# Performance work log

Measured on AMD Instinct MI355X. Metric: run time of the kernel, lower is better.

The kernel has to match this reference:

```python
import jax, jax.numpy as jnp
import numpy as np

B, M, F, E = 64, 1024, 4, 256      # batch, memory length, tokens-per-memory-cell, emb_size
NW, HOPS, PL = 32000, 3, 128       # vocab, hops, profile_len


def _embed(table, idx):
    # nn.Embedding with padding_idx=0 -> index 0 maps to zero vector
    return table[idx] * (idx != 0)[..., None].astype(table.dtype)


def _gru_step(x, h, Wih, Whh, bih, bhh):
    # single-step PyTorch GRU cell
    gi = x @ Wih.T + bih
    gh = h @ Whh.T + bhh
    ir, iz, i_n = jnp.split(gi, 3, axis=-1)
    hr, hz, h_n = jnp.split(gh, 3, axis=-1)
    r = jax.nn.sigmoid(ir + hr)
    z = jax.nn.sigmoid(iz + hz)
    n = jnp.tanh(i_n + r * h_n)
    return (1.0 - z) * n + z * h


def setup_inputs() -> dict:
    key = jax.random.key(0)
    ks = jax.random.split(key, 13)
    # HOPS+1 unique embedding tables: A[0..hops-1] plus C[hops-1]; C[h]=tables[h+1] (weight tying)
    tables = (jax.random.normal(ks[0], (HOPS + 1, NW, E)) * 0.1).at[:, 0, :].set(0.0)
    s = 1.0 / np.sqrt(E)
    Wih = jax.random.uniform(ks[1], (3 * E, E), minval=-s, maxval=s)
    Whh = jax.random.uniform(ks[2], (3 * E, E), minval=-s, maxval=s)
    bih = jax.random.uniform(ks[3], (3 * E,), minval=-s, maxval=s)
    bhh = jax.random.uniform(ks[4], (3 * E,), minval=-s, maxval=s)
    sp = 1.0 / np.sqrt(PL)
    Wp = jax.random.uniform(ks[5], (E, PL), minval=-sp, maxval=sp)
    bp = jax.random.uniform(ks[6], (E,), minval=-sp, maxval=sp)
    sv = 1.0 / np.sqrt(2 * E)
    Wv = jax.random.uniform(ks[7], (NW, 2 * E), minval=-sv, maxval=sv)
    bv = jax.random.uniform(ks[8], (NW,), minval=-sv, maxval=sv)
    context = jax.random.randint(ks[9], (B, M, F), 0, NW)
    y_ = jax.random.randint(ks[10], (B,), 0, NW)
    h_ = jax.random.normal(ks[11], (1, B, E))
    profile_encoding = jax.random.normal(ks[12], (B, PL))
    return dict(tables=tables, Wih=Wih, Whh=Whh, bih=bih, bhh=bhh, Wp=Wp, bp=bp,
                Wv=Wv, bv=bv, context=context, y_=y_, h_=h_,
                profile_encoding=profile_encoding)


def reference(tables, Wih, Whh, bih, bhh, Wp, bp, Wv, bv, context, y_, h_, profile_encoding):
    # load_memory (eval mode: no word dropout): memories[h] = sum over F of table[h] embeddings
    ctx = context.reshape(B, M * F)
    mems = [_embed(tables[hop], ctx).reshape(B, M, F, E).sum(axis=2) for hop in range(HOPS + 1)]
    # decoder step
    m = _embed(tables[1], y_)                    # C[0](y_)
    h = _gru_step(m, h_[0], Wih, Whh, bih, bhh)  # [B, E]
    q = h
    p = p_vocab = p_resto = None
    for hop in range(HOPS):
        p_ = mems[hop] * q[:, None, :]           # [B, M, E] elementwise attention scores
        p = p_.sum(axis=2)                        # [B, M]
        attn = jax.nn.softmax(p, axis=1)
        o = jnp.einsum('bm,bme->be', attn, mems[hop + 1])
        if hop == 0:
            p_vocab = jnp.concatenate([h, o], axis=1) @ Wv.T + bv  # uses q[0]=h
        if hop == 1:
            enc = profile_encoding @ Wp.T + bp   # [B, E]
            p_resto = jnp.einsum('bme,be->bm', p_, enc)
        q = q + o
    return p, p_vocab, p_resto, h[None]          # p_ptr, p_vocab, p_resto, h [1,B,E]
```

## Files before the change

### kernel.cpp

```cpp
#include <hip/hip_runtime.h>
#include <cstdint>

#define B_ 64
#define M_ 1024
#define F_ 4
#define E_ 256
#define NW_ 32000
#define PL_ 128

#define P_OFF   0
#define PV_OFF  65536
#define PR_OFF  2113536
#define H_OFF   2179072

typedef unsigned short u16;
typedef unsigned int u32;

typedef __bf16 bf16x8 __attribute__((ext_vector_type(8)));
typedef float f32x4 __attribute__((ext_vector_type(4)));

__device__ __forceinline__ u16 f2bf(float f) {
    u32 x = __builtin_bit_cast(u32, f);
    u32 r = (x + 0x7fffu + ((x >> 16) & 1u)) >> 16;
    return (u16)r;
}
__device__ __forceinline__ float bflo(u32 v) {
    return __builtin_bit_cast(float, v << 16);
}
__device__ __forceinline__ float bfhi(u32 v) {
    return __builtin_bit_cast(float, v & 0xffff0000u);
}
__device__ __forceinline__ float dot8(uint4 u, float4 qa, float4 qb) {
    return bflo(u.x) * qa.x + bfhi(u.x) * qa.y + bflo(u.y) * qa.z + bfhi(u.y) * qa.w +
           bflo(u.z) * qb.x + bfhi(u.z) * qb.y + bflo(u.w) * qb.z + bfhi(u.w) * qb.w;
}
__device__ __forceinline__ void acc8(uint4 u, float* a) {
    a[0] += bflo(u.x); a[1] += bfhi(u.x); a[2] += bflo(u.y); a[3] += bfhi(u.y);
    a[4] += bflo(u.z); a[5] += bfhi(u.z); a[6] += bflo(u.w); a[7] += bfhi(u.w);
}
__device__ __forceinline__ uint4 pack8(const float* s) {
    uint4 u;
    u.x = (u32)f2bf(s[0]) | ((u32)f2bf(s[1]) << 16);
    u.y = (u32)f2bf(s[2]) | ((u32)f2bf(s[3]) << 16);
    u.z = (u32)f2bf(s[4]) | ((u32)f2bf(s[5]) << 16);
    u.w = (u32)f2bf(s[6]) | ((u32)f2bf(s[7]) << 16);
    return u;
}
__device__ __forceinline__ bf16x8 pack_bf8(float4 a, float4 b) {
    union { u16 s[8]; bf16x8 v; } u;
    u.s[0] = f2bf(a.x); u.s[1] = f2bf(a.y); u.s[2] = f2bf(a.z); u.s[3] = f2bf(a.w);
    u.s[4] = f2bf(b.x); u.s[5] = f2bf(b.y); u.s[6] = f2bf(b.z); u.s[7] = f2bf(b.w);
    return u.v;
}

__global__ __launch_bounds__(256) void k_conv(
    const float* __restrict__ tables, u16* __restrict__ t0b, u16* __restrict__ t12)
{
    int t = blockIdx.y;
    int c = blockIdx.x * 256 + threadIdx.x;
    const float* src = tables + (size_t)t * NW_ * E_ + (size_t)c * 8;
    float4 a = *(const float4*)src;
    float4 b = *(const float4*)(src + 4);
    float s[8] = {a.x, a.y, a.z, a.w, b.x, b.y, b.z, b.w};
    uint4 u = pack8(s);
    if (t == 0) {
        *(uint4*)(t0b + (size_t)c * 8) = u;
    } else {
        int row = c >> 5, e = (c & 31) * 8;
        *(uint4*)(t12 + (size_t)row * 512 + (t - 1) * 256 + e) = u;
    }
}

__global__ __launch_bounds__(256) void k_gru(
    const float* __restrict__ tables, const float* __restrict__ Wih,
    const float* __restrict__ Whh, const float* __restrict__ bih,
    const float* __restrict__ bhh, const float* __restrict__ Wp,
    const float* __restrict__ bp, const int* __restrict__ y,
    const float* __restrict__ h_, const float* __restrict__ pe,
    float* __restrict__ q0, float* __restrict__ enc, float* __restrict__ outh)
{
    int b = blockIdx.x, t = threadIdx.x;
    __shared__ float m_s[E_], h_s[E_], pe_s[PL_];
    int yb = y[b];
    m_s[t] = tables[(size_t)NW_ * E_ + (size_t)yb * E_ + t];
    h_s[t] = h_[b * E_ + t];
    if (t < PL_) pe_s[t] = pe[b * PL_ + t];
    __syncthreads();

    float g_i[3], g_h[3];
#pragma unroll
    for (int g = 0; g < 3; g++) {
        int j = g * E_ + t;
        float ai = bih[j], ah = bhh[j];
        const float4* wi = (const float4*)(Wih + (size_t)j * E_);
        const float4* wh = (const float4*)(Whh + (size_t)j * E_);
#pragma unroll 8
        for (int e = 0; e < E_ / 4; e++) {
            float4 a = wi[e], c = wh[e];
            ai += a.x * m_s[4 * e] + a.y * m_s[4 * e + 1] +
                  a.z * m_s[4 * e + 2] + a.w * m_s[4 * e + 3];
            ah += c.x * h_s[4 * e] + c.y * h_s[4 * e + 1] +
                  c.z * h_s[4 * e + 2] + c.w * h_s[4 * e + 3];
        }
        g_i[g] = ai; g_h[g] = ah;
    }
    float r = 1.f / (1.f + expf(-(g_i[0] + g_h[0])));
    float z = 1.f / (1.f + expf(-(g_i[1] + g_h[1])));
    float n = tanhf(g_i[2] + r * g_h[2]);
    float hv = (1.f - z) * n + z * h_s[t];
    q0[b * E_ + t] = hv;
    outh[b * E_ + t] = hv;

    float ea = bp[t];
    const float4* wp = (const float4*)(Wp + (size_t)t * PL_);
#pragma unroll 8
    for (int p = 0; p < PL_ / 4; p++) {
        float4 a = wp[p];
        ea += a.x * pe_s[4 * p] + a.y * pe_s[4 * p + 1] +
              a.z * pe_s[4 * p + 2] + a.w * pe_s[4 * p + 3];
    }
    enc[b * E_ + t] = ea;
}

__global__ __launch_bounds__(256) void k_scores0(
    const u16* __restrict__ t0b, const int* __restrict__ ctx,
    const float* __restrict__ q, float* __restrict__ p_ws)
{
    int b = blockIdx.y, grp = blockIdx.x;
    int lane = threadIdx.x & 63, w = threadIdx.x >> 6;
    int h = lane >> 5, l32 = lane & 31, e0 = l32 * 8;
    float4 qa = *(const float4*)(q + b * E_ + e0);
    float4 qb = *(const float4*)(q + b * E_ + e0 + 4);
    int mbase = grp * 32 + w * 8;
    const int4* cp = (const int4*)(ctx + ((size_t)b * M_ + mbase) * 4);
    int4 c[8];
#pragma unroll
    for (int i = 0; i < 8; i++) c[i] = cp[i];

    float pa[8];
#pragma unroll
    for (int i = 0; i < 8; i++) {
        int ia = h ? c[i].y : c[i].x;
        int ib = h ? c[i].w : c[i].z;
        uint4 ra = *(const uint4*)(t0b + (size_t)ia * E_ + e0);
        uint4 rb = *(const uint4*)(t0b + (size_t)ib * E_ + e0);
        pa[i] = dot8(ra, qa, qb) + dot8(rb, qa, qb);
    }
#pragma unroll
    for (int o = 32; o > 0; o >>= 1)
#pragma unroll
        for (int i = 0; i < 8; i++) pa[i] += __shfl_xor(pa[i], o, 64);
    if (lane == 0)
#pragma unroll
        for (int i = 0; i < 8; i++) p_ws[(size_t)b * M_ + mbase + i] = pa[i];
}

__global__ __launch_bounds__(256) void k_soft(
    float* __restrict__ p_ws, const float* __restrict__ qcur,
    float* __restrict__ qnext)
{
    int b = blockIdx.x, t = threadIdx.x;
    __shared__ float red[256];
    float4 v = *(const float4*)(p_ws + (size_t)b * M_ + t * 4);
    float lm = fmaxf(fmaxf(v.x, v.y), fmaxf(v.z, v.w));
    red[t] = lm;
    __syncthreads();
    for (int s = 128; s > 0; s >>= 1) {
        if (t < s) red[t] = fmaxf(red[t], red[t + s]);
        __syncthreads();
    }
    float mx = red[0];
    __syncthreads();
    float e0 = expf(v.x - mx), e1 = expf(v.y - mx);
    float e2 = expf(v.z - mx), e3 = expf(v.w - mx);
    red[t] = e0 + e1 + e2 + e3;
    __syncthreads();
    for (int s = 128; s > 0; s >>= 1) {
        if (t < s) red[t] += red[t + s];
        __syncthreads();
    }
    float inv = 1.f / red[0];
    float4 o = make_float4(e0 * inv, e1 * inv, e2 * inv, e3 * inv);
    *(float4*)(p_ws + (size_t)b * M_ + t * 4) = o;
    qnext[b * E_ + t] = qcur[b * E_ + t];
}

__global__ __launch_bounds__(256) void k_mems12(
    const u16* __restrict__ t12, const int* __restrict__ ctx,
    const float* __restrict__ attn0, u16* __restrict__ mems1,
    u16* __restrict__ mems2, float* __restrict__ q1)
{
    int b = blockIdx.y, grp = blockIdx.x;
    int lane = threadIdx.x & 63, w = threadIdx.x >> 6;
    int h = lane >> 5, l32 = lane & 31, e0 = l32 * 8;
    int mbase = grp * 32 + w * 8;
    const int4* cp = (const int4*)(ctx + ((size_t)b * M_ + mbase) * 4);
    int4 c[8];
#pragma unroll
    for (int i = 0; i < 8; i++) c[i] = cp[i];
    float4 a01 = *(const float4*)(attn0 + (size_t)b * M_ + mbase);
    float4 a23 = *(const float4*)(attn0 + (size_t)b * M_ + mbase + 4);
    float wg[8] = {a01.x, a01.y, a01.z, a01.w, a23.x, a23.y, a23.z, a23.w};

    u16* mout = h ? mems2 : mems1;
    float o_acc[8] = {0, 0, 0, 0, 0, 0, 0, 0};
#pragma unroll
    for (int i = 0; i < 8; i++) {
        size_t off = (size_t)h * 256 + e0;
        uint4 r0 = *(const uint4*)(t12 + (size_t)c[i].x * 512 + off);
        uint4 r1 = *(const uint4*)(t12 + (size_t)c[i].y * 512 + off);
        uint4 r2 = *(const uint4*)(t12 + (size_t)c[i].z * 512 + off);
        uint4 r3 = *(const uint4*)(t12 + (size_t)c[i].w * 512 + off);
        float acc[8] = {0, 0, 0, 0, 0, 0, 0, 0};
        acc8(r0, acc); acc8(r1, acc); acc8(r2, acc); acc8(r3, acc);
        *(uint4*)(mout + ((size_t)(b * M_ + mbase + i)) * 256 + e0) = pack8(acc);
        if (h == 0) {
            float wgt = wg[i];
#pragma unroll
            for (int j = 0; j < 8; j++) o_acc[j] += wgt * acc[j];
        }
    }
    __shared__ float red[4][E_];
    if (h == 0)
#pragma unroll
        for (int j = 0; j < 8; j++) red[w][e0 + j] = o_acc[j];
    __syncthreads();
    int t = threadIdx.x;
    float s = red[0][t] + red[1][t] + red[2][t] + red[3][t];
    atomicAdd(q1 + b * E_ + t, s);
}

template <int MODE>
__global__ __launch_bounds__(256) void k_sscores(
    const u16* __restrict__ mems, const float* __restrict__ q,
    const float* __restrict__ enc, float* __restrict__ p_ws,
    float* __restrict__ out)
{
    int b = blockIdx.y, grp = blockIdx.x;
    int lane = threadIdx.x & 63, w = threadIdx.x >> 6;
    int h = lane >> 5, l32 = lane & 31, e0 = l32 * 8;
    float4 qa = *(const float4*)(q + b * E_ + e0);
    float4 qb = *(const float4*)(q + b * E_ + e0 + 4);
    float4 ea4 = make_float4(0, 0, 0, 0), eb4 = make_float4(0, 0, 0, 0);
    if (MODE == 1) {
        float4 ev = *(const float4*)(enc + b * E_ + e0);
        float4 ew = *(const float4*)(enc + b * E_ + e0 + 4);
        ea4 = make_float4(qa.x * ev.x, qa.y * ev.y, qa.z * ev.z, qa.w * ev.w);
        eb4 = make_float4(qb.x * ew.x, qb.y * ew.y, qb.z * ew.z, qb.w * ew.w);
    }
    int mbase = grp * 32 + w * 8;
    float pa[4], pr[4];
#pragma unroll
    for (int i = 0; i < 4; i++) {
        int m = mbase + 2 * i + h;
        uint4 r = *(const uint4*)(mems + ((size_t)(b * M_ + m)) * 256 + e0);
        pa[i] = dot8(r, qa, qb);
        if (MODE == 1) pr[i] = dot8(r, ea4, eb4);
    }
#pragma unroll
    for (int o = 16; o > 0; o >>= 1)
#pragma unroll
        for (int i = 0; i < 4; i++) {
            pa[i] += __shfl_xor(pa[i], o, 64);
            if (MODE == 1) pr[i] += __shfl_xor(pr[i], o, 64);
        }
    if (l32 == 0) {
#pragma unroll
        for (int i = 0; i < 4; i++) {
            int m = mbase + 2 * i + h;
            if (MODE == 2) out[P_OFF + (size_t)b * M_ + m] = pa[i];
            else           p_ws[(size_t)b * M_ + m] = pa[i];
            if (MODE == 1) out[PR_OFF + (size_t)b * M_ + m] = pr[i];
        }
    }
}

__global__ __launch_bounds__(256) void k_so(
    const u16* __restrict__ mems, const float* __restrict__ attn,
    float* __restrict__ qnext)
{
    int b = blockIdx.y, ch = blockIdx.x;
    int lane = threadIdx.x & 63, w = threadIdx.x >> 6;
    int h = lane >> 5, l32 = lane & 31, e0 = l32 * 8;
    int m0 = ch * 128;
    float acc[8] = {0, 0, 0, 0, 0, 0, 0, 0};
    for (int i = 0; i < 16; i++) {
        int m = m0 + i * 8 + w * 2 + h;
        float wgt = attn[(size_t)b * M_ + m];
        uint4 r = *(const uint4*)(mems + ((size_t)(b * M_ + m)) * 256 + e0);
        acc[0] += wgt * bflo(r.x); acc[1] += wgt * bfhi(r.x);
        acc[2] += wgt * bflo(r.y); acc[3] += wgt * bfhi(r.y);
        acc[4] += wgt * bflo(r.z); acc[5] += wgt * bfhi(r.z);
        acc[6] += wgt * bflo(r.w); acc[7] += wgt * bfhi(r.w);
    }
    __shared__ float red[8][E_];
    int hw = threadIdx.x >> 5;
#pragma unroll
    for (int j = 0; j < 8; j++) red[hw][e0 + j] = acc[j];
    __syncthreads();
    int t = threadIdx.x;
    float s = 0.f;
#pragma unroll
    for (int k = 0; k < 8; k++) s += red[k][t];
    atomicAdd(qnext + b * E_ + t, s);
}

__global__ __launch_bounds__(256) void k_pvocab(
    const float* __restrict__ Wv, const float* __restrict__ bv,
    const float* __restrict__ q0, const float* __restrict__ q1,
    float* __restrict__ out)
{
    __shared__ u16 X[64 * 512];
    int t = threadIdx.x;
#pragma unroll
    for (int it = 0; it < 16; it++) {
        int id = t + it * 256;
        int bb = id >> 6, c = id & 63;
        float v[8];
        if (c < 32) {
            const float* s = q0 + bb * E_ + c * 8;
#pragma unroll
            for (int j = 0; j < 8; j++) v[j] = s[j];
        } else {
            const float* s1 = q1 + bb * E_ + (c - 32) * 8;
            const float* s0 = q0 + bb * E_ + (c - 32) * 8;
#pragma unroll
            for (int j = 0; j < 8; j++) v[j] = s1[j] - s0[j];
        }
        uint4 uv = pack8(v);
        *(uint4*)(&X[bb * 512 + ((c ^ (bb & 7)) << 3)]) = uv;
    }
    __syncthreads();

    int lane = t & 63, w = t >> 6;
    int n0 = blockIdx.x * 128 + w * 32;
    int l15 = lane & 15, quad = lane >> 4;
    f32x4 acc[4][2];
#pragma unroll
    for (int mt = 0; mt < 4; mt++)
#pragma unroll
        for (int nt = 0; nt < 2; nt++)
            acc[mt][nt] = f32x4{0.f, 0.f, 0.f, 0.f};

    for (int ks = 0; ks < 16; ks++) {
        bf16x8 a[4], bfr[2];
#pragma unroll
        for (int mt = 0; mt < 4; mt++) {
            int m = mt * 16 + l15;
            int c = ks * 4 + quad;
            a[mt] = *(const bf16x8*)(&X[m * 512 + ((c ^ (m & 7)) << 3)]);
        }
#pragma unroll
        for (int nt = 0; nt < 2; nt++) {
            int n = n0 + nt * 16 + l15;
            const float4* wp = (const float4*)(Wv + (size_t)n * 512 + ks * 32 + quad * 8);
            bfr[nt] = pack_bf8(wp[0], wp[1]);
        }
#pragma unroll
        for (int mt = 0; mt < 4; mt++)
#pragma unroll
            for (int nt = 0; nt < 2; nt++)
                acc[mt][nt] = __builtin_amdgcn_mfma_f32_16x16x32_bf16(
                    a[mt], bfr[nt], acc[mt][nt], 0, 0, 0);
    }
#pragma unroll
    for (int nt = 0; nt < 2; nt++) {
        int n = n0 + nt * 16 + l15;
        float bvv = bv[n];
#pragma unroll
        for (int mt = 0; mt < 4; mt++) {
#pragma unroll
            for (int j = 0; j < 4; j++) {
                int m = mt * 16 + quad * 4 + j;
                out[PV_OFF + (size_t)m * 32000 + n] = acc[mt][nt][j] + bvv;
            }
        }
    }
}

extern "C" void kernel_launch(void* const* d_in, const int* in_sizes, int n_in,
                              void* d_out, int out_size, void* d_ws, size_t ws_size,
                              hipStream_t stream)
{
    const float* tables = (const float*)d_in[0];
    const float* Wih = (const float*)d_in[1];
    const float* Whh = (const float*)d_in[2];
    const float* bih = (const float*)d_in[3];
    const float* bhh = (const float*)d_in[4];
    const float* Wp  = (const float*)d_in[5];
    const float* bp  = (const float*)d_in[6];
    const float* Wv  = (const float*)d_in[7];
    const float* bv  = (const float*)d_in[8];
    const int* ctx = (const int*)d_in[9];
    const int* y   = (const int*)d_in[10];
    const float* h_  = (const float*)d_in[11];
    const float* pe  = (const float*)d_in[12];
    float* out = (float*)d_out;

    float* Wf   = (float*)d_ws;
    float* q    = Wf;
    float* enc  = Wf + 65536;
    float* p_ws = Wf + 81920;
    char* base  = (char*)d_ws + 589824;
    u16* t0b    = (u16*)base;
    u16* t12    = (u16*)(base + 16384000);
    u16* mems1  = (u16*)(base + 16384000 + 32768000);
    u16* mems2  = (u16*)(base + 16384000 + 32768000 + 33554432);

    k_conv<<<dim3(4000, 3), 256, 0, stream>>>(tables, t0b, t12);
    k_gru<<<64, 256, 0, stream>>>(tables, Wih, Whh, bih, bhh, Wp, bp, y, h_, pe,
                                  q, enc, out + H_OFF);
    k_scores0<<<dim3(32, 64), 256, 0, stream>>>(t0b, ctx, q, p_ws);
    k_soft<<<64, 256, 0, stream>>>(p_ws, q, q + 16384);
    k_mems12<<<dim3(32, 64), 256, 0, stream>>>(t12, ctx, p_ws, mems1, mems2,
                                               q + 16384);
    k_sscores<1><<<dim3(32, 64), 256, 0, stream>>>(mems1, q + 16384, enc, p_ws, out);
    k_soft<<<64, 256, 0, stream>>>(p_ws, q + 16384, q + 32768);
    k_so<<<dim3(8, 64), 256, 0, stream>>>(mems2, p_ws, q + 32768);
    k_sscores<2><<<dim3(32, 64), 256, 0, stream>>>(mems2, q + 32768, enc, p_ws, out);
    k_pvocab<<<250, 256, 0, stream>>>(Wv, bv, q, q + 16384, out);
}
```

Measured before the change: 399.5 us.

## Merge independent kernels into shared launches via block-index dispatch

Folds the table-conversion kernel and the GRU kernel into one launch whose first 64 blocks run the GRU and whose remaining blocks convert tables. Also merges the p_vocab MFMA GEMM into the hop-1 scores kernel, so the two independent pieces of work run concurrently in one grid. This removes two launches and lets small, low-occupancy kernels overlap with bandwidth-bound work. The cost is that the combined kernels carry the larger LDS footprint of the GEMM path, which may lower occupancy for the score blocks.

New measurement: 370.3 us. 1.08x faster.

```diff
diff --git a/kernel.cpp b/kernel.cpp
--- a/kernel.cpp
+++ b/kernel.cpp
@@ -53,33 +53,34 @@
     return u.v;
 }
 
-__global__ __launch_bounds__(256) void k_conv(
-    const float* __restrict__ tables, u16* __restrict__ t0b, u16* __restrict__ t12)
-{
-    int t = blockIdx.y;
-    int c = blockIdx.x * 256 + threadIdx.x;
-    const float* src = tables + (size_t)t * NW_ * E_ + (size_t)c * 8;
-    float4 a = *(const float4*)src;
-    float4 b = *(const float4*)(src + 4);
-    float s[8] = {a.x, a.y, a.z, a.w, b.x, b.y, b.z, b.w};
-    uint4 u = pack8(s);
-    if (t == 0) {
-        *(uint4*)(t0b + (size_t)c * 8) = u;
-    } else {
-        int row = c >> 5, e = (c & 31) * 8;
-        *(uint4*)(t12 + (size_t)row * 512 + (t - 1) * 256 + e) = u;
-    }
-}
-
-__global__ __launch_bounds__(256) void k_gru(
+__global__ __launch_bounds__(256) void k_convgru(
     const float* __restrict__ tables, const float* __restrict__ Wih,
     const float* __restrict__ Whh, const float* __restrict__ bih,
     const float* __restrict__ bhh, const float* __restrict__ Wp,
     const float* __restrict__ bp, const int* __restrict__ y,
     const float* __restrict__ h_, const float* __restrict__ pe,
-    float* __restrict__ q0, float* __restrict__ enc, float* __restrict__ outh)
-{
-    int b = blockIdx.x, t = threadIdx.x;
+    float* __restrict__ q0, float* __restrict__ enc, float* __restrict__ outh,
+    u16* __restrict__ t0b, u16* __restrict__ t12)
+{
+    int vb = blockIdx.x, tid = threadIdx.x;
+    if (vb >= 64) {
+        int cvb = vb - 64;
+        int t = cvb / 4000;
+        int c = (cvb % 4000) * 256 + tid;
+        const float* src = tables + (size_t)t * NW_ * E_ + (size_t)c * 8;
+        float4 a = *(const float4*)src;
+        float4 b = *(const float4*)(src + 4);
+        float s[8] = {a.x, a.y, a.z, a.w, b.x, b.y, b.z, b.w};
+        uint4 u = pack8(s);
+        if (t == 0) {
+            *(uint4*)(t0b + (size_t)c * 8) = u;
+        } else {
+            int row = c >> 5, e = (c & 31) * 8;
+            *(uint4*)(t12 + (size_t)row * 512 + (t - 1) * 256 + e) = u;
+        }
+        return;
+    }
+    int b = vb, t = tid;
     __shared__ float m_s[E_], h_s[E_], pe_s[PL_];
     int yb = y[b];
     m_s[t] = tables[(size_t)NW_ * E_ + (size_t)yb * E_ + t];
@@ -230,10 +231,119 @@
     atomicAdd(q1 + b * E_ + t, s);
 }
 
-template <int MODE>
-__global__ __launch_bounds__(256) void k_sscores(
+__global__ __launch_bounds__(256) void k_ss1pv(
+    const u16* __restrict__ mems, const float* __restrict__ q1v,
+    const float* __restrict__ enc, float* __restrict__ p_ws,
+    float* __restrict__ out, const float* __restrict__ Wv,
+    const float* __restrict__ bv, const float* __restrict__ q0)
+{
+    if (blockIdx.x >= 250) {
+        int vb = blockIdx.x - 250;
+        int grp = vb & 31, b = vb >> 5;
+        int lane = threadIdx.x & 63, w = threadIdx.x >> 6;
+        int h = lane >> 5, l32 = lane & 31, e0 = l32 * 8;
+        float4 qa = *(const float4*)(q1v + b * E_ + e0);
+        float4 qb = *(const float4*)(q1v + b * E_ + e0 + 4);
+        float4 ev = *(const float4*)(enc + b * E_ + e0);
+        float4 ew = *(const float4*)(enc + b * E_ + e0 + 4);
+        float4 ea4 = make_float4(qa.x * ev.x, qa.y * ev.y, qa.z * ev.z, qa.w * ev.w);
+        float4 eb4 = make_float4(qb.x * ew.x, qb.y * ew.y, qb.z * ew.z, qb.w * ew.w);
+        int mbase = grp * 32 + w * 8;
+        float pa[4], pr[4];
+#pragma unroll
+        for (int i = 0; i < 4; i++) {
+            int m = mbase + 2 * i + h;
+            uint4 r = *(const uint4*)(mems + ((size_t)(b * M_ + m)) * 256 + e0);
+            pa[i] = dot8(r, qa, qb);
+            pr[i] = dot8(r, ea4, eb4);
+        }
+#pragma unroll
+        for (int o = 16; o > 0; o >>= 1)
+#pragma unroll
+            for (int i = 0; i < 4; i++) {
+                pa[i] += __shfl_xor(pa[i], o, 64);
+                pr[i] += __shfl_xor(pr[i], o, 64);
+            }
+        if (l32 == 0) {
+#pragma unroll
+            for (int i = 0; i < 4; i++) {
+                int m = mbase + 2 * i + h;
+                p_ws[(size_t)b * M_ + m] = pa[i];
+                out[PR_OFF + (size_t)b * M_ + m] = pr[i];
+            }
+        }
+        return;
+    }
+    __shared__ u16 X[64 * 512];
+    int t = threadIdx.x;
+#pragma unroll
+    for (int it = 0; it < 16; it++) {
+        int id = t + it * 256;
+        int bb = id >> 6, c = id & 63;
+        float v[8];
+        if (c < 32) {
+            const float* s = q0 + bb * E_ + c * 8;
+#pragma unroll
+            for (int j = 0; j < 8; j++) v[j] = s[j];
+        } else {
+            const float* s1 = q1v + bb * E_ + (c - 32) * 8;
+            const float* s0 = q0 + bb * E_ + (c - 32) * 8;
+#pragma unroll
+            for (int j = 0; j < 8; j++) v[j] = s1[j] - s0[j];
+        }
+        uint4 uv = pack8(v);
+        *(uint4*)(&X[bb * 512 + ((c ^ (bb & 7)) << 3)]) = uv;
+    }
+    __syncthreads();
+
+    int lane = t & 63, w = t >> 6;
+    int n0 = blockIdx.x * 128 + w * 32;
+    int l15 = lane & 15, quad = lane >> 4;
+    f32x4 acc[4][2];
+#pragma unroll
+    for (int mt = 0; mt < 4; mt++)
+#pragma unroll
+        for (int nt = 0; nt < 2; nt++)
+            acc[mt][nt] = f32x4{0.f, 0.f, 0.f, 0.f};
+
+    for (int ks = 0; ks < 16; ks++) {
+        bf16x8 a[4], bfr[2];
+#pragma unroll
+        for (int mt = 0; mt < 4; mt++) {
+            int m = mt * 16 + l15;
+            int c = ks * 4 + quad;
+            a[mt] = *(const bf16x8*)(&X[m * 512 + ((c ^ (m & 7)) << 3)]);
+        }
+#pragma unroll
+        for (int nt = 0; nt < 2; nt++) {
+            int n = n0 + nt * 16 + l15;
+            const float4* wp = (const float4*)(Wv + (size_t)n * 512 + ks * 32 + quad * 8);
+            bfr[nt] = pack_bf8(wp[0], wp[1]);
+        }
+#pragma unroll
+        for (int mt = 0; mt < 4; mt++)
+#pragma unroll
+            for (int nt = 0; nt < 2; nt++)
+                acc[mt][nt] = __builtin_amdgcn_mfma_f32_16x16x32_bf16(
+                    a[mt], bfr[nt], acc[mt][nt], 0, 0, 0);
+    }
+#pragma unroll
+    for (int nt = 0; nt < 2; nt++) {
+        int n = n0 + nt * 16 + l15;
+        float bvv = bv[n];
+#pragma unroll
+        for (int mt = 0; mt < 4; mt++) {
+#pragma unroll
+            for (int j = 0; j < 4; j++) {
+                int m = mt * 16 + quad * 4 + j;
+                out[PV_OFF + (size_t)m * 32000 + n] = acc[mt][nt][j] + bvv;
+            }
+        }
+    }
+}
+
+__global__ __launch_bounds__(256) void k_sscores2(
     const u16* __restrict__ mems, const float* __restrict__ q,
-    const float* __restrict__ enc, float* __restrict__ p_ws,
     float* __restrict__ out)
 {
     int b = blockIdx.y, grp = blockIdx.x;
@@ -241,36 +351,23 @@
     int h = lane >> 5, l32 = lane & 31, e0 = l32 * 8;
     float4 qa = *(const float4*)(q + b * E_ + e0);
     float4 qb = *(const float4*)(q + b * E_ + e0 + 4);
-    float4 ea4 = make_float4(0, 0, 0, 0), eb4 = make_float4(0, 0, 0, 0);
-    if (MODE == 1) {
-        float4 ev = *(const float4*)(enc + b * E_ + e0);
-        float4 ew = *(const float4*)(enc + b * E_ + e0 + 4);
-        ea4 = make_float4(qa.x * ev.x, qa.y * ev.y, qa.z * ev.z, qa.w * ev.w);
-        eb4 = make_float4(qb.x * ew.x, qb.y * ew.y, qb.z * ew.z, qb.w * ew.w);
-    }
     int mbase = grp * 32 + w * 8;
-    float pa[4], pr[4];
+    float pa[4];
 #pragma unroll
     for (int i = 0; i < 4; i++) {
         int m = mbase + 2 * i + h;
         uint4 r = *(const uint4*)(mems + ((size_t)(b * M_ + m)) * 256 + e0);
         pa[i] = dot8(r, qa, qb);
-        if (MODE == 1) pr[i] = dot8(r, ea4, eb4);
     }
 #pragma unroll
     for (int o = 16; o > 0; o >>= 1)
 #pragma unroll
-        for (int i = 0; i < 4; i++) {
-            pa[i] += __shfl_xor(pa[i], o, 64);
-            if (MODE == 1) pr[i] += __shfl_xor(pr[i], o, 64);
-        }
+        for (int i = 0; i < 4; i++) pa[i] += __shfl_xor(pa[i], o, 64);
     if (l32 == 0) {
 #pragma unroll
         for (int i = 0; i < 4; i++) {
             int m = mbase + 2 * i + h;
-            if (MODE == 2) out[P_OFF + (size_t)b * M_ + m] = pa[i];
-            else           p_ws[(size_t)b * M_ + m] = pa[i];
-            if (MODE == 1) out[PR_OFF + (size_t)b * M_ + m] = pr[i];
+            out[P_OFF + (size_t)b * M_ + m] = pa[i];
         }
     }
 }
@@ -303,79 +400,6 @@
 #pragma unroll
     for (int k = 0; k < 8; k++) s += red[k][t];
     atomicAdd(qnext + b * E_ + t, s);
-}
-
-__global__ __launch_bounds__(256) void k_pvocab(
-    const float* __restrict__ Wv, const float* __restrict__ bv,
-    const float* __restrict__ q0, const float* __restrict__ q1,
-    float* __restrict__ out)
-{
-    __shared__ u16 X[64 * 512];
-    int t = threadIdx.x;
-#pragma unroll
-    for (int it = 0; it < 16; it++) {
-        int id = t + it * 256;
-        int bb = id >> 6, c = id & 63;
-        float v[8];
-        if (c < 32) {
-            const float* s = q0 + bb * E_ + c * 8;
-#pragma unroll
-            for (int j = 0; j < 8; j++) v[j] = s[j];
-        } else {
-            const float* s1 = q1 + bb * E_ + (c - 32) * 8;
-            const float* s0 = q0 + bb * E_ + (c - 32) * 8;
-#pragma unroll
-            for (int j = 0; j < 8; j++) v[j] = s1[j] - s0[j];
-        }
-        uint4 uv = pack8(v);
-        *(uint4*)(&X[bb * 512 + ((c ^ (bb & 7)) << 3)]) = uv;
-    }
-    __syncthreads();
-
-    int lane = t & 63, w = t >> 6;
-    int n0 = blockIdx.x * 128 + w * 32;
-    int l15 = lane & 15, quad = lane >> 4;
-    f32x4 acc[4][2];
-#pragma unroll
-    for (int mt = 0; mt < 4; mt++)
-#pragma unroll
-        for (int nt = 0; nt < 2; nt++)
-            acc[mt][nt] = f32x4{0.f, 0.f, 0.f, 0.f};
-
-    for (int ks = 0; ks < 16; ks++) {
-        bf16x8 a[4], bfr[2];
-#pragma unroll
-        for (int mt = 0; mt < 4; mt++) {
-            int m = mt * 16 + l15;
-            int c = ks * 4 + quad;
-            a[mt] = *(const bf16x8*)(&X[m * 512 + ((c ^ (m & 7)) << 3)]);
-        }
-#pragma unroll
-        for (int nt = 0; nt < 2; nt++) {
-            int n = n0 + nt * 16 + l15;
-            const float4* wp = (const float4*)(Wv + (size_t)n * 512 + ks * 32 + quad * 8);
-            bfr[nt] = pack_bf8(wp[0], wp[1]);
-        }
-#pragma unroll
-        for (int mt = 0; mt < 4; mt++)
-#pragma unroll
-            for (int nt = 0; nt < 2; nt++)
-                acc[mt][nt] = __builtin_amdgcn_mfma_f32_16x16x32_bf16(
-                    a[mt], bfr[nt], acc[mt][nt], 0, 0, 0);
-    }
-#pragma unroll
-    for (int nt = 0; nt < 2; nt++) {
-        int n = n0 + nt * 16 + l15;
-        float bvv = bv[n];
-#pragma unroll
-        for (int mt = 0; mt < 4; mt++) {
-#pragma unroll
-            for (int j = 0; j < 4; j++) {
-                int m = mt * 16 + quad * 4 + j;
-                out[PV_OFF + (size_t)m * 32000 + n] = acc[mt][nt][j] + bvv;
-            }
-        }
-    }
 }
 
 extern "C" void kernel_launch(void* const* d_in, const int* in_sizes, int n_in,
@@ -407,16 +431,16 @@
     u16* mems1  = (u16*)(base + 16384000 + 32768000);
     u16* mems2  = (u16*)(base + 16384000 + 32768000 + 33554432);
 
-    k_conv<<<dim3(4000, 3), 256, 0, stream>>>(tables, t0b, t12);
-    k_gru<<<64, 256, 0, stream>>>(tables, Wih, Whh, bih, bhh, Wp, bp, y, h_, pe,
-                                  q, enc, out + H_OFF);
+    k_convgru<<<12064, 256, 0, stream>>>(tables, Wih, Whh, bih, bhh, Wp, bp,
+                                         y, h_, pe, q, enc, out + H_OFF,
+                                         t0b, t12);
     k_scores0<<<dim3(32, 64), 256, 0, stream>>>(t0b, ctx, q, p_ws);
     k_soft<<<64, 256, 0, stream>>>(p_ws, q, q + 16384);
     k_mems12<<<dim3(32, 64), 256, 0, stream>>>(t12, ctx, p_ws, mems1, mems2,
                                                q + 16384);
-    k_sscores<1><<<dim3(32, 64), 256, 0, stream>>>(mems1, q + 16384, enc, p_ws, out);
+    k_ss1pv<<<2298, 256, 0, stream>>>(mems1, q + 16384, enc, p_ws, out,
+                                      Wv, bv, q);
     k_soft<<<64, 256, 0, stream>>>(p_ws, q + 16384, q + 32768);
     k_so<<<dim3(8, 64), 256, 0, stream>>>(mems2, p_ws, q + 32768);
-    k_sscores<2><<<dim3(32, 64), 256, 0, stream>>>(mems2, q + 32768, enc, p_ws, out);
-    k_pvocab<<<250, 256, 0, stream>>>(Wv, bv, q, q + 16384, out);
-}
+    k_sscores2<<<dim3(32, 64), 256, 0, stream>>>(mems2, q + 32768, out);
+}
```
